# Performance work log

Hardware: AMD Instinct MI355X
Metric: run time of the kernel (lower is better)

Reference implementation:

```python
import jax, jax.numpy as jnp
import numpy as np

D_MODEL = 256      # cfg.d_model
D_INPUT = 64       # cfg.d_input == n_bands
MEM = 10           # cfg.memory_length
NSYNC = 32         # cfg.n_synch_out
ITERS = 2          # cfg.iterations (internal CTM ticks per audio frame)
VOCAB = 15
MINW = 16          # SynapseUNET minimum width; depth=2 -> widths [256, 16]
MHD = 2            # memory_hidden_dims
SYNC_DIM = NSYNC * (NSYNC + 1) // 2  # 528 upper-tri pairwise products


def _ln(x, g, b, eps=1e-5):
    m = x.mean(-1, keepdims=True)
    v = ((x - m) ** 2).mean(-1, keepdims=True)
    return (x - m) * jax.lax.rsqrt(v + eps) * g + b


def _glu(x):
    a, b = jnp.split(x, 2, axis=-1)
    return a * jax.nn.sigmoid(b)


def setup_inputs() -> dict:
    key = jax.random.key(0)
    ks = iter(jax.random.split(key, 40))
    def rn(shape, fan_in):
        return jax.random.uniform(next(ks), shape, jnp.float32, -1.0, 1.0) / np.sqrt(fan_in)
    B, T = 16, 1500
    z = jnp.zeros
    o = jnp.ones
    return {
        "batch_features": jax.random.normal(next(ks), (B, T, D_INPUT), jnp.float32),
        # learned initial traces
        "start_trace": rn((D_MODEL, MEM), MEM),
        "start_activated_trace": rn((D_MODEL, MEM), MEM),
        # classic-control backbone: Linear(64->64) + ReLU
        "Wb": rn((D_INPUT, D_INPUT), D_INPUT), "bb": z((D_INPUT,)),
        # SynapseUNET depth=2, widths [256,16]; input dim = d_input + d_model = 320
        "Wf": rn((D_INPUT + D_MODEL, 2 * D_MODEL), D_INPUT + D_MODEL), "bf": z((2 * D_MODEL,)),
        "gf": o((D_MODEL,)), "bef": z((D_MODEL,)),
        "Wd": rn((D_MODEL, 2 * MINW), D_MODEL), "bd": z((2 * MINW,)),
        "gd": o((MINW,)), "bed": z((MINW,)),
        "Wu": rn((MINW, 2 * D_MODEL), MINW), "bu": z((2 * D_MODEL,)),
        "gu": o((D_MODEL,)), "beu": z((D_MODEL,)),
        "gs": o((D_MODEL,)), "bes": z((D_MODEL,)),
        # deep neuron-level models (per-neuron MLP over the memory trace)
        "w1": rn((MEM, D_MODEL, 2 * MHD), MEM), "b1": z((1, D_MODEL, 2 * MHD)),
        "w2": rn((MHD, D_MODEL, 2), MHD), "b2": z((1, D_MODEL, 2)),
        # output head Linear(528 -> 15)
        "Wh": rn((SYNC_DIM, VOCAB), SYNC_DIM), "bh": z((VOCAB,)),
    }


def reference(batch_features, start_trace, start_activated_trace, Wb, bb,
              Wf, bf, gf, bef, Wd, bd, gd, bed, Wu, bu, gu, beu, gs, bes,
              w1, b1, w2, b2, Wh, bh):
    B = batch_features.shape[0]
    iu, ju = np.triu_indices(NSYNC)  # static index pattern (528 pairs)

    st0 = jnp.broadcast_to(start_trace, (B, D_MODEL, MEM))
    ast0 = jnp.broadcast_to(start_activated_trace, (B, D_MODEL, MEM))

    def synapses(x):  # (B, 320) -> (B, 256), U-Net with one down/up level
        h0 = _ln(_glu(x @ Wf + bf), gf, bef)        # (B, 256)
        d1 = _ln(_glu(h0 @ Wd + bd), gd, bed)       # (B, 16)
        u0 = _ln(_glu(d1 @ Wu + bu), gu, beu)       # (B, 256)
        return _ln(u0 + h0, gs, bes)                # skip + LN

    def nlm(trace):  # per-neuron MLP over memory: (B, 256, 10) -> (B, 256)
        h = _glu(jnp.einsum('bdm,mdh->bdh', trace, w1) + b1)  # (B, 256, 2)
        h = _glu(jnp.einsum('bdm,mdh->bdh', h, w2) + b2)      # (B, 256, 1)
        return h[..., 0]

    def step(carry, x_t):
        st, ast = carry
        kv = jax.nn.relu(x_t @ Wb + bb)  # backbone features (B, 64)
        act = ast[:, :, -1]
        for _ in range(ITERS):  # internal CTM ticks (fixed, small)
            pre = jnp.concatenate([kv, act], axis=-1)             # (B, 320)
            state = synapses(pre)                                  # (B, 256)
            st = jnp.concatenate([st[:, :, 1:], state[:, :, None]], axis=-1)
            act = nlm(st)                                          # (B, 256)
            ast = jnp.concatenate([ast[:, :, 1:], act[:, :, None]], axis=-1)
        sel = act[:, :NSYNC]  # 'first-last': out-sync uses first n_synch_out neurons
        sync = (sel[:, :, None] * sel[:, None, :])[:, iu, ju]      # (B, 528)
        return (st, ast), sync @ Wh + bh                            # (B, 15)

    _, logits = jax.lax.scan(step, (st0, ast0), jnp.swapaxes(batch_features, 0, 1))
    return jnp.swapaxes(logits, 0, 1)  # (B, T, vocab)
```

## Files before the change

### kernel.cpp

```cpp
#include <hip/hip_runtime.h>
#include <math.h>

#define T_LEN 1500
#define DM 256
#define DI 64
#define MEMN 10
#define SYNCD 528
#define VOC 15

typedef _Float16 f16x2 __attribute__((ext_vector_type(2)));
typedef _Float16 f16x8 __attribute__((ext_vector_type(8)));

#define FDOT2(a, b, c) __builtin_amdgcn_fdot2((a), (b), (c), false)

static __device__ __forceinline__ float dot8(f16x8 w, f16x8 q, float acc) {
  acc = FDOT2(__builtin_shufflevector(w, w, 0, 1), __builtin_shufflevector(q, q, 0, 1), acc);
  acc = FDOT2(__builtin_shufflevector(w, w, 2, 3), __builtin_shufflevector(q, q, 2, 3), acc);
  acc = FDOT2(__builtin_shufflevector(w, w, 4, 5), __builtin_shufflevector(q, q, 4, 5), acc);
  acc = FDOT2(__builtin_shufflevector(w, w, 6, 7), __builtin_shufflevector(q, q, 6, 7), acc);
  return acc;
}
static __device__ __forceinline__ f16x2 pack2(float a, float b) {
  f16x2 r; r.x = (_Float16)a; r.y = (_Float16)b; return r;
}
static __device__ __forceinline__ float sigm(float x) { return 1.0f / (1.0f + __expf(-x)); }

struct Params {
  const float *x, *st0, *ast0, *Wb, *bb, *Wf, *bf, *gf, *bef,
              *Wd, *bd, *gd, *bed, *Wu, *bu, *gu, *beu, *gs, *bes,
              *w1, *b1, *w2, *b2, *Wh, *bh;
  float* out;
};

struct Smem {
  float4 W1v[MEMN * DM];
  float4 W2v[DM];
  float4 B1v[DM];
  float2 B2v[DM];
  float Bf[2 * DM];
  float Bu[2 * DM];
  float Bd[32];
  float Gf[DM], Bef[DM], Gu[DM], Beu[DM], Gs[DM], Bes[DM];
  float Gd[16], Bed[16];
  float Bh[16];
  float Bb[DI];
  __attribute__((aligned(16))) float St[MEMN * DM];
  __attribute__((aligned(16))) float H0[DM];
  float Act[DM];
  __attribute__((aligned(16))) float D1[16];
  float X2[2][DI];
  __attribute__((aligned(16))) f16x2 Pre2[160];
  float PartD[16 * 33];
  float PartK[512];
  float PartH[240];
  float2 RedAB[8];
  float2 Red2AB[8];
  float Prod[SYNCD];
  float WhL[SYNCD * VOC];
  int Pair[SYNCD];
};

#define FOR20(X) X(0) X(1) X(2) X(3) X(4) X(5) X(6) X(7) X(8) X(9) \
                 X(10) X(11) X(12) X(13) X(14) X(15) X(16) X(17) X(18) X(19)

#define DECLW(i) f16x8 wa##i, wb##i;
#define LOADW(i) { const float* Wc = P.Wf + (size_t)(p160 + (i) * 8) * 512 + ch; \
  f16x8 ta, tb; \
  _Pragma("unroll") for (int e = 0; e < 8; ++e) { \
    ta[e] = (_Float16)Wc[e * 512]; tb[e] = (_Float16)Wc[e * 512 + 256]; } \
  wa##i = ta; wb##i = tb; }
#define DOT0(i) { f16x8 q = pr8[i]; aA0 = dot8(wa##i, q, aA0); aB0 = dot8(wb##i, q, aB0); }
#define DOT1(i) { f16x8 q = pr8[i]; aA1 = dot8(wa##i, q, aA1); aB1 = dot8(wb##i, q, aB1); }
#define DOTSEQ DOT0(0) DOT1(1) DOT0(2) DOT1(3) DOT0(4) DOT1(5) DOT0(6) DOT1(7) DOT0(8) DOT1(9) \
               DOT0(10) DOT1(11) DOT0(12) DOT1(13) DOT0(14) DOT1(15) DOT0(16) DOT1(17) DOT0(18) DOT1(19)

__global__ __launch_bounds__(512) __attribute__((amdgpu_waves_per_eu(1, 2)))
void ctm_kernel(Params P) {
  const int tid = threadIdx.x;
  const int b = blockIdx.x;
  extern __shared__ char smraw[];
  Smem* sm = (Smem*)smraw;

  for (int i = tid; i < MEMN * DM; i += 512) sm->W1v[i] = ((const float4*)P.w1)[i];
  if (tid < DM) {
    float2 a = ((const float2*)P.w2)[tid];
    float2 c = ((const float2*)P.w2)[DM + tid];
    float4 w; w.x = a.x; w.y = a.y; w.z = c.x; w.w = c.y;
    sm->W2v[tid] = w;
    sm->B1v[tid] = ((const float4*)P.b1)[tid];
    sm->B2v[tid] = ((const float2*)P.b2)[tid];
    sm->Gf[tid] = P.gf[tid]; sm->Bef[tid] = P.bef[tid];
    sm->Gu[tid] = P.gu[tid]; sm->Beu[tid] = P.beu[tid];
    sm->Gs[tid] = P.gs[tid]; sm->Bes[tid] = P.bes[tid];
  }
  sm->Bf[tid] = P.bf[tid];
  sm->Bu[tid] = P.bu[tid];
  if (tid < 32) sm->Bd[tid] = P.bd[tid];
  if (tid < 16) { sm->Gd[tid] = P.gd[tid]; sm->Bed[tid] = P.bed[tid]; }
  if (tid < VOC) sm->Bh[tid] = P.bh[tid];
  if (tid < DI) sm->Bb[tid] = P.bb[tid];
  for (int i = tid; i < MEMN * DM; i += 512) {
    int m = i >> 8, d = i & 255;
    sm->St[m * DM + d] = P.st0[d * MEMN + m];
  }
  if (tid < DI) sm->X2[0][tid] = P.x[(size_t)b * T_LEN * DI + tid];
  for (int i = tid; i < SYNCD * VOC; i += 512) sm->WhL[i] = P.Wh[i];
  for (int pp = tid; pp < SYNCD; pp += 512) {
    int i = 0, cum = 0;
    while (pp >= cum + (32 - i)) { cum += 32 - i; ++i; }
    sm->Pair[pp] = (i << 8) | (i + (pp - cum));
  }

  const int p = tid & 1;
  const int ch = tid >> 1;
  const int p160 = p * 160;
  FOR20(DECLW)
  FOR20(LOADW)
  const int jD = tid & 31, kcD = tid >> 5;
  float wd[16];
  #pragma unroll
  for (int q = 0; q < 16; ++q) wd[q] = P.Wd[(kcD * 16 + q) * 32 + jD];
  float wua[8], wub[8];
  #pragma unroll
  for (int q = 0; q < 8; ++q) {
    wua[q] = P.Wu[(p * 8 + q) * 512 + ch];
    wub[q] = P.Wu[(p * 8 + q) * 512 + ch + 256];
  }
  const int jK = tid & 63, kcK = tid >> 6;
  float wbr[8];
  #pragma unroll
  for (int q = 0; q < 8; ++q) wbr[q] = P.Wb[(kcK * 8 + q) * 64 + jK];

  __syncthreads();

  {
    float s = 0.f;
    #pragma unroll
    for (int q = 0; q < 8; ++q) s += sm->X2[0][kcK * 8 + q] * wbr[q];
    sm->PartK[kcK * 64 + jK] = s;
    if ((tid & 3) == 0) {
      int e = tid >> 2;
      float a0 = P.ast0[(2 * e) * MEMN + (MEMN - 1)];
      float a1 = P.ast0[(2 * e + 1) * MEMN + (MEMN - 1)];
      sm->Pre2[32 + e] = pack2(a0, a1);
    }
  }
  __syncthreads();
  if (tid >= 256 && tid < 320) {
    int j = tid - 256;
    float kv = sm->Bb[j];
    #pragma unroll
    for (int kc = 0; kc < 8; ++kc) kv += sm->PartK[kc * 64 + j];
    kv = fmaxf(kv, 0.f);
    float kn = __shfl_xor(kv, 1);
    if ((j & 1) == 0) sm->Pre2[j >> 1] = pack2(kv, kn);
  }
  __syncthreads();

  int head = 0;
  for (int t = 0; t < T_LEN; ++t) {
    float xr = 0.f;
    if (tid < DI && t + 1 < T_LEN) xr = P.x[((size_t)b * T_LEN + (t + 1)) * DI + tid];

    for (int it = 0; it < 2; ++it) {
      if (it == 1 && tid < DI) sm->X2[(t + 1) & 1][tid] = xr;
      float aA0 = 0.f, aA1 = 0.f, aB0 = 0.f, aB1 = 0.f;
      const f16x8* pr8 = (const f16x8*)(sm->Pre2 + p * 80);
      DOTSEQ
      float av = aA0 + aA1, bv = aB0 + aB1;
      av += __shfl_xor(av, 1); bv += __shfl_xor(bv, 1);
      av += sm->Bf[ch]; bv += sm->Bf[DM + ch];
      float g = av * sigm(bv);
      float s1 = g, s2 = g * g;
      #pragma unroll
      for (int m = 1; m < 64; m <<= 1) { s1 += __shfl_xor(s1, m); s2 += __shfl_xor(s2, m); }
      if ((tid & 63) == 0) { float2 r; r.x = s1; r.y = s2; sm->RedAB[tid >> 6] = r; }
      __syncthreads();

      float S1 = 0.f, S2 = 0.f;
      #pragma unroll
      for (int w = 0; w < 8; ++w) { float2 r = sm->RedAB[w]; S1 += r.x; S2 += r.y; }
      float mean = S1 * (1.0f / 512.0f);
      float var = S2 * (1.0f / 512.0f) - mean * mean;
      float h0v = (g - mean) * rsqrtf(var + 1e-5f) * sm->Gf[ch] + sm->Bef[ch];
      if (!p) sm->H0[ch] = h0v;
      __syncthreads();

      {
        float s = 0.f;
        #pragma unroll
        for (int qq = 0; qq < 4; ++qq) {
          float4 hv = ((const float4*)sm->H0)[kcD * 4 + qq];
          s += hv.x * wd[qq * 4 + 0] + hv.y * wd[qq * 4 + 1]
             + hv.z * wd[qq * 4 + 2] + hv.w * wd[qq * 4 + 3];
        }
        sm->PartD[kcD * 33 + jD] = s;
      }
      __syncthreads();

      if (tid < 32) {
        int j = tid & 15;
        int half = tid >> 4;
        float s = 0.f;
        #pragma unroll
        for (int kc = 0; kc < 16; ++kc) s += sm->PartD[kc * 33 + half * 16 + j];
        float oth = __shfl_xor(s, 16);
        float gg = (s + sm->Bd[j]) * sigm(oth + sm->Bd[16 + j]);
        float t1 = gg, t2 = gg * gg;
        #pragma unroll
        for (int m = 1; m < 16; m <<= 1) { t1 += __shfl_xor(t1, m); t2 += __shfl_xor(t2, m); }
        float mn = t1 * (1.0f / 16.0f), vr = t2 * (1.0f / 16.0f) - mn * mn;
        float d1 = (gg - mn) * rsqrtf(vr + 1e-5f) * sm->Gd[j] + sm->Bed[j];
        if (tid < 16) sm->D1[j] = d1;
      }
      __syncthreads();

      float gu;
      {
        const float4* d4 = (const float4*)sm->D1;
        float4 dl = d4[p * 2], dh = d4[p * 2 + 1];
        float ua = dl.x * wua[0] + dl.y * wua[1] + dl.z * wua[2] + dl.w * wua[3]
                 + dh.x * wua[4] + dh.y * wua[5] + dh.z * wua[6] + dh.w * wua[7];
        float ub = dl.x * wub[0] + dl.y * wub[1] + dl.z * wub[2] + dl.w * wub[3]
                 + dh.x * wub[4] + dh.y * wub[5] + dh.z * wub[6] + dh.w * wub[7];
        ua += __shfl_xor(ua, 1); ub += __shfl_xor(ub, 1);
        ua += sm->Bu[ch]; ub += sm->Bu[DM + ch];
        gu = ua * sigm(ub);
        float t1 = gu, t2 = gu * gu;
        #pragma unroll
        for (int m = 1; m < 64; m <<= 1) { t1 += __shfl_xor(t1, m); t2 += __shfl_xor(t2, m); }
        if ((tid & 63) == 0) { float2 r; r.x = t1; r.y = t2; sm->RedAB[tid >> 6] = r; }
      }
      __syncthreads();

      float x2v;
      {
        float U1 = 0.f, U2 = 0.f;
        #pragma unroll
        for (int w = 0; w < 8; ++w) { float2 r = sm->RedAB[w]; U1 += r.x; U2 += r.y; }
        float mn = U1 * (1.0f / 512.0f), vr = U2 * (1.0f / 512.0f) - mn * mn;
        float u0 = (gu - mn) * rsqrtf(vr + 1e-5f) * sm->Gu[ch] + sm->Beu[ch];
        x2v = u0 + h0v;
        float t1 = x2v, t2 = x2v * x2v;
        #pragma unroll
        for (int m = 1; m < 64; m <<= 1) { t1 += __shfl_xor(t1, m); t2 += __shfl_xor(t2, m); }
        if ((tid & 63) == 0) { float2 r; r.x = t1; r.y = t2; sm->Red2AB[tid >> 6] = r; }
      }
      __syncthreads();

      {
        float V1 = 0.f, V2 = 0.f;
        #pragma unroll
        for (int w = 0; w < 8; ++w) { float2 r = sm->Red2AB[w]; V1 += r.x; V2 += r.y; }
        float mn = V1 * (1.0f / 512.0f), vr = V2 * (1.0f / 512.0f) - mn * mn;
        float state = (x2v - mn) * rsqrtf(vr + 1e-5f) * sm->Gs[ch] + sm->Bes[ch];
        if (!p) sm->St[head * DM + ch] = state;
        float4 h1 = sm->B1v[ch];
        int base = head + 1; if (base >= MEMN) base -= MEMN;
        #pragma unroll
        for (int m = 0; m < MEMN - 1; ++m) {
          int slot = base + m; if (slot >= MEMN) slot -= MEMN;
          float tr = sm->St[slot * DM + ch];
          float4 wv = sm->W1v[m * DM + ch];
          h1.x += tr * wv.x; h1.y += tr * wv.y; h1.z += tr * wv.z; h1.w += tr * wv.w;
        }
        {
          float4 wv = sm->W1v[(MEMN - 1) * DM + ch];
          h1.x += state * wv.x; h1.y += state * wv.y; h1.z += state * wv.z; h1.w += state * wv.w;
        }
        float g0 = h1.x * sigm(h1.z), g1 = h1.y * sigm(h1.w);
        float4 w2v = sm->W2v[ch];
        float2 b2v = sm->B2v[ch];
        float o0 = g0 * w2v.x + g1 * w2v.z + b2v.x;
        float o1 = g0 * w2v.y + g1 * w2v.w + b2v.y;
        float act = o0 * sigm(o1);
        if (!p) sm->Act[ch] = act;
        float an = __shfl_xor(act, 2);
        if ((tid & 3) == 0) sm->Pre2[32 + (tid >> 2)] = pack2(act, an);
        head += 1; if (head >= MEMN) head = 0;
      }
      __syncthreads();
    }

    {
      int pr = sm->Pair[tid];
      sm->Prod[tid] = sm->Act[pr >> 8] * sm->Act[pr & 255];
      if (tid < SYNCD - 512) {
        int pr2 = sm->Pair[512 + tid];
        sm->Prod[512 + tid] = sm->Act[pr2 >> 8] * sm->Act[pr2 & 255];
      }
      const float* X = sm->X2[(t + 1) & 1];
      float s = 0.f;
      #pragma unroll
      for (int q = 0; q < 8; ++q) s += X[kcK * 8 + q] * wbr[q];
      sm->PartK[kcK * 64 + jK] = s;
      if (t > 0 && tid < VOC) {
        float o = sm->Bh[tid];
        #pragma unroll
        for (int kc2 = 0; kc2 < 16; ++kc2) o += sm->PartH[kc2 * 15 + tid];
        P.out[((size_t)b * T_LEN + (t - 1)) * VOC + tid] = o;
      }
    }
    __syncthreads();

    if (tid < 240) {
      int kc = (tid * 4370) >> 16;
      int v = tid - kc * 15;
      float s = 0.f;
      #pragma unroll
      for (int q = 0; q < 33; ++q) {
        int pp = kc * 33 + q;
        s += sm->Prod[pp] * sm->WhL[pp * 15 + v];
      }
      sm->PartH[kc * 15 + v] = s;
    } else if (tid >= 256 && tid < 320) {
      int j = tid - 256;
      float kv = sm->Bb[j];
      #pragma unroll
      for (int kc = 0; kc < 8; ++kc) kv += sm->PartK[kc * 64 + j];
      kv = fmaxf(kv, 0.f);
      float kn = __shfl_xor(kv, 1);
      if ((j & 1) == 0) sm->Pre2[j >> 1] = pack2(kv, kn);
    }
    __syncthreads();
  }

  if (tid < VOC) {
    float o = sm->Bh[tid];
    #pragma unroll
    for (int kc = 0; kc < 16; ++kc) o += sm->PartH[kc * 15 + tid];
    P.out[((size_t)b * T_LEN + (T_LEN - 1)) * VOC + tid] = o;
  }
}

extern "C" void kernel_launch(void* const* d_in, const int* in_sizes, int n_in,
                              void* d_out, int out_size, void* d_ws, size_t ws_size,
                              hipStream_t stream) {
  (void)d_ws; (void)ws_size; (void)n_in; (void)out_size;
  Params P;
  P.x   = (const float*)d_in[0];
  P.st0 = (const float*)d_in[1];
  P.ast0= (const float*)d_in[2];
  P.Wb  = (const float*)d_in[3];
  P.bb  = (const float*)d_in[4];
  P.Wf  = (const float*)d_in[5];
  P.bf  = (const float*)d_in[6];
  P.gf  = (const float*)d_in[7];
  P.bef = (const float*)d_in[8];
  P.Wd  = (const float*)d_in[9];
  P.bd  = (const float*)d_in[10];
  P.gd  = (const float*)d_in[11];
  P.bed = (const float*)d_in[12];
  P.Wu  = (const float*)d_in[13];
  P.bu  = (const float*)d_in[14];
  P.gu  = (const float*)d_in[15];
  P.beu = (const float*)d_in[16];
  P.gs  = (const float*)d_in[17];
  P.bes = (const float*)d_in[18];
  P.w1  = (const float*)d_in[19];
  P.b1  = (const float*)d_in[20];
  P.w2  = (const float*)d_in[21];
  P.b2  = (const float*)d_in[22];
  P.Wh  = (const float*)d_in[23];
  P.bh  = (const float*)d_in[24];
  P.out = (float*)d_out;

  int B = in_sizes[0] / (T_LEN * DI);
  hipFuncSetAttribute((const void*)ctm_kernel, hipFuncAttributeMaxDynamicSharedMemorySize,
                      (int)sizeof(Smem));
  hipLaunchKernelGGL(ctm_kernel, dim3(B), dim3(512), sizeof(Smem), stream, P);
}
```

Baseline: 14.41 ms.

## Double block size to 1024 threads, split each channel's work across four lanes

Each 256-channel synapse row is now split across 4 lanes instead of 2, with the block grown to 1024 threads. Every thread therefore holds half as many Wf f16 weights in registers, and the block-wide reductions and partial-sum arrays are resized to 16 waves. The backbone Wb weights move from registers into shared memory. This shortens the serial per-thread dot-product chain in a latency-bound, sequential-over-time kernel. In exchange it adds extra shuffle reduction steps, more waves taking part in each of the many per-step barriers, and more LDS traffic for Wb.

```diff
diff --git a/kernel.cpp b/kernel.cpp
--- a/kernel.cpp
+++ b/kernel.cpp
@@ -44,44 +44,43 @@
   float Gd[16], Bed[16];
   float Bh[16];
   float Bb[DI];
+  float WbL[DI * DI];
   __attribute__((aligned(16))) float St[MEMN * DM];
   __attribute__((aligned(16))) float H0[DM];
   float Act[DM];
   __attribute__((aligned(16))) float D1[16];
   float X2[2][DI];
   __attribute__((aligned(16))) f16x2 Pre2[160];
-  float PartD[16 * 33];
-  float PartK[512];
+  float PartD[32 * 33];
+  float PartK[16 * 64];
   float PartH[240];
-  float2 RedAB[8];
-  float2 Red2AB[8];
+  float2 RedAB[16];
+  float2 Red2AB[16];
   float Prod[SYNCD];
   float WhL[SYNCD * VOC];
   int Pair[SYNCD];
 };
 
-#define FOR20(X) X(0) X(1) X(2) X(3) X(4) X(5) X(6) X(7) X(8) X(9) \
-                 X(10) X(11) X(12) X(13) X(14) X(15) X(16) X(17) X(18) X(19)
+#define FOR10(X) X(0) X(1) X(2) X(3) X(4) X(5) X(6) X(7) X(8) X(9)
 
 #define DECLW(i) f16x8 wa##i, wb##i;
-#define LOADW(i) { const float* Wc = P.Wf + (size_t)(p160 + (i) * 8) * 512 + ch; \
+#define LOADW(i) { const float* Wc = P.Wf + (size_t)(q80 + (i) * 8) * 512 + ch; \
   f16x8 ta, tb; \
   _Pragma("unroll") for (int e = 0; e < 8; ++e) { \
     ta[e] = (_Float16)Wc[e * 512]; tb[e] = (_Float16)Wc[e * 512 + 256]; } \
   wa##i = ta; wb##i = tb; }
-#define DOT0(i) { f16x8 q = pr8[i]; aA0 = dot8(wa##i, q, aA0); aB0 = dot8(wb##i, q, aB0); }
-#define DOT1(i) { f16x8 q = pr8[i]; aA1 = dot8(wa##i, q, aA1); aB1 = dot8(wb##i, q, aB1); }
-#define DOTSEQ DOT0(0) DOT1(1) DOT0(2) DOT1(3) DOT0(4) DOT1(5) DOT0(6) DOT1(7) DOT0(8) DOT1(9) \
-               DOT0(10) DOT1(11) DOT0(12) DOT1(13) DOT0(14) DOT1(15) DOT0(16) DOT1(17) DOT0(18) DOT1(19)
-
-__global__ __launch_bounds__(512) __attribute__((amdgpu_waves_per_eu(1, 2)))
+#define DOT0(i) { f16x8 qq_ = pr8[i]; aA0 = dot8(wa##i, qq_, aA0); aB0 = dot8(wb##i, qq_, aB0); }
+#define DOT1(i) { f16x8 qq_ = pr8[i]; aA1 = dot8(wa##i, qq_, aA1); aB1 = dot8(wb##i, qq_, aB1); }
+#define DOTSEQ DOT0(0) DOT1(1) DOT0(2) DOT1(3) DOT0(4) DOT1(5) DOT0(6) DOT1(7) DOT0(8) DOT1(9)
+
+__global__ __launch_bounds__(1024)
 void ctm_kernel(Params P) {
   const int tid = threadIdx.x;
   const int b = blockIdx.x;
   extern __shared__ char smraw[];
   Smem* sm = (Smem*)smraw;
 
-  for (int i = tid; i < MEMN * DM; i += 512) sm->W1v[i] = ((const float4*)P.w1)[i];
+  for (int i = tid; i < MEMN * DM; i += 1024) sm->W1v[i] = ((const float4*)P.w1)[i];
   if (tid < DM) {
     float2 a = ((const float2*)P.w2)[tid];
     float2 c = ((const float2*)P.w2)[DM + tid];
@@ -93,64 +92,60 @@
     sm->Gu[tid] = P.gu[tid]; sm->Beu[tid] = P.beu[tid];
     sm->Gs[tid] = P.gs[tid]; sm->Bes[tid] = P.bes[tid];
   }
-  sm->Bf[tid] = P.bf[tid];
-  sm->Bu[tid] = P.bu[tid];
+  if (tid < 2 * DM) { sm->Bf[tid] = P.bf[tid]; sm->Bu[tid] = P.bu[tid]; }
   if (tid < 32) sm->Bd[tid] = P.bd[tid];
   if (tid < 16) { sm->Gd[tid] = P.gd[tid]; sm->Bed[tid] = P.bed[tid]; }
   if (tid < VOC) sm->Bh[tid] = P.bh[tid];
   if (tid < DI) sm->Bb[tid] = P.bb[tid];
-  for (int i = tid; i < MEMN * DM; i += 512) {
+  for (int i = tid; i < DI * DI; i += 1024) sm->WbL[i] = P.Wb[i];
+  for (int i = tid; i < MEMN * DM; i += 1024) {
     int m = i >> 8, d = i & 255;
     sm->St[m * DM + d] = P.st0[d * MEMN + m];
   }
   if (tid < DI) sm->X2[0][tid] = P.x[(size_t)b * T_LEN * DI + tid];
-  for (int i = tid; i < SYNCD * VOC; i += 512) sm->WhL[i] = P.Wh[i];
-  for (int pp = tid; pp < SYNCD; pp += 512) {
+  if (tid < 128) {
+    float a0 = P.ast0[(2 * tid) * MEMN + (MEMN - 1)];
+    float a1 = P.ast0[(2 * tid + 1) * MEMN + (MEMN - 1)];
+    sm->Pre2[32 + tid] = pack2(a0, a1);
+  }
+  for (int i = tid; i < SYNCD * VOC; i += 1024) sm->WhL[i] = P.Wh[i];
+  for (int pp = tid; pp < SYNCD; pp += 1024) {
     int i = 0, cum = 0;
     while (pp >= cum + (32 - i)) { cum += 32 - i; ++i; }
     sm->Pair[pp] = (i << 8) | (i + (pp - cum));
   }
 
-  const int p = tid & 1;
-  const int ch = tid >> 1;
-  const int p160 = p * 160;
-  FOR20(DECLW)
-  FOR20(LOADW)
+  const int q = tid & 3;
+  const int ch = tid >> 2;
+  const int q80 = q * 80;
+  FOR10(DECLW)
+  FOR10(LOADW)
   const int jD = tid & 31, kcD = tid >> 5;
-  float wd[16];
+  float wd[8];
   #pragma unroll
-  for (int q = 0; q < 16; ++q) wd[q] = P.Wd[(kcD * 16 + q) * 32 + jD];
-  float wua[8], wub[8];
+  for (int i = 0; i < 8; ++i) wd[i] = P.Wd[(kcD * 8 + i) * 32 + jD];
+  float wua[4], wub[4];
   #pragma unroll
-  for (int q = 0; q < 8; ++q) {
-    wua[q] = P.Wu[(p * 8 + q) * 512 + ch];
-    wub[q] = P.Wu[(p * 8 + q) * 512 + ch + 256];
+  for (int i = 0; i < 4; ++i) {
+    wua[i] = P.Wu[(q * 4 + i) * 512 + ch];
+    wub[i] = P.Wu[(q * 4 + i) * 512 + ch + 256];
   }
   const int jK = tid & 63, kcK = tid >> 6;
-  float wbr[8];
-  #pragma unroll
-  for (int q = 0; q < 8; ++q) wbr[q] = P.Wb[(kcK * 8 + q) * 64 + jK];
 
   __syncthreads();
 
   {
     float s = 0.f;
     #pragma unroll
-    for (int q = 0; q < 8; ++q) s += sm->X2[0][kcK * 8 + q] * wbr[q];
+    for (int i = 0; i < 4; ++i) s += sm->X2[0][kcK * 4 + i] * sm->WbL[(kcK * 4 + i) * 64 + jK];
     sm->PartK[kcK * 64 + jK] = s;
-    if ((tid & 3) == 0) {
-      int e = tid >> 2;
-      float a0 = P.ast0[(2 * e) * MEMN + (MEMN - 1)];
-      float a1 = P.ast0[(2 * e + 1) * MEMN + (MEMN - 1)];
-      sm->Pre2[32 + e] = pack2(a0, a1);
-    }
   }
   __syncthreads();
   if (tid >= 256 && tid < 320) {
     int j = tid - 256;
     float kv = sm->Bb[j];
     #pragma unroll
-    for (int kc = 0; kc < 8; ++kc) kv += sm->PartK[kc * 64 + j];
+    for (int kc = 0; kc < 16; ++kc) kv += sm->PartK[kc * 64 + j];
     kv = fmaxf(kv, 0.f);
     float kn = __shfl_xor(kv, 1);
     if ((j & 1) == 0) sm->Pre2[j >> 1] = pack2(kv, kn);
@@ -165,10 +160,11 @@
     for (int it = 0; it < 2; ++it) {
       if (it == 1 && tid < DI) sm->X2[(t + 1) & 1][tid] = xr;
       float aA0 = 0.f, aA1 = 0.f, aB0 = 0.f, aB1 = 0.f;
-      const f16x8* pr8 = (const f16x8*)(sm->Pre2 + p * 80);
+      const f16x8* pr8 = (const f16x8*)sm->Pre2 + q * 10;
       DOTSEQ
       float av = aA0 + aA1, bv = aB0 + aB1;
-      av += __shfl_xor(av, 1); bv += __shfl_xor(bv, 1);
+      av += __shfl_xor(av, 1); av += __shfl_xor(av, 2);
+      bv += __shfl_xor(bv, 1); bv += __shfl_xor(bv, 2);
       av += sm->Bf[ch]; bv += sm->Bf[DM + ch];
       float g = av * sigm(bv);
       float s1 = g, s2 = g * g;
@@ -179,18 +175,18 @@
 
       float S1 = 0.f, S2 = 0.f;
       #pragma unroll
-      for (int w = 0; w < 8; ++w) { float2 r = sm->RedAB[w]; S1 += r.x; S2 += r.y; }
-      float mean = S1 * (1.0f / 512.0f);
-      float var = S2 * (1.0f / 512.0f) - mean * mean;
+      for (int w = 0; w < 16; ++w) { float2 r = sm->RedAB[w]; S1 += r.x; S2 += r.y; }
+      float mean = S1 * (1.0f / 1024.0f);
+      float var = S2 * (1.0f / 1024.0f) - mean * mean;
       float h0v = (g - mean) * rsqrtf(var + 1e-5f) * sm->Gf[ch] + sm->Bef[ch];
-      if (!p) sm->H0[ch] = h0v;
+      if (q == 0) sm->H0[ch] = h0v;
       __syncthreads();
 
       {
         float s = 0.f;
         #pragma unroll
-        for (int qq = 0; qq < 4; ++qq) {
-          float4 hv = ((const float4*)sm->H0)[kcD * 4 + qq];
+        for (int qq = 0; qq < 2; ++qq) {
+          float4 hv = ((const float4*)sm->H0)[kcD * 2 + qq];
           s += hv.x * wd[qq * 4 + 0] + hv.y * wd[qq * 4 + 1]
              + hv.z * wd[qq * 4 + 2] + hv.w * wd[qq * 4 + 3];
         }
@@ -198,12 +194,14 @@
       }
       __syncthreads();
 
-      if (tid < 32) {
+      if (tid < 64) {
+        int col = tid & 31;
+        int kh = tid >> 5;
         int j = tid & 15;
-        int half = tid >> 4;
         float s = 0.f;
         #pragma unroll
-        for (int kc = 0; kc < 16; ++kc) s += sm->PartD[kc * 33 + half * 16 + j];
+        for (int i = 0; i < 16; ++i) s += sm->PartD[(kh * 16 + i) * 33 + col];
+        s += __shfl_xor(s, 32);
         float oth = __shfl_xor(s, 16);
         float gg = (s + sm->Bd[j]) * sigm(oth + sm->Bd[16 + j]);
         float t1 = gg, t2 = gg * gg;
@@ -217,13 +215,11 @@
 
       float gu;
       {
-        const float4* d4 = (const float4*)sm->D1;
-        float4 dl = d4[p * 2], dh = d4[p * 2 + 1];
-        float ua = dl.x * wua[0] + dl.y * wua[1] + dl.z * wua[2] + dl.w * wua[3]
-                 + dh.x * wua[4] + dh.y * wua[5] + dh.z * wua[6] + dh.w * wua[7];
-        float ub = dl.x * wub[0] + dl.y * wub[1] + dl.z * wub[2] + dl.w * wub[3]
-                 + dh.x * wub[4] + dh.y * wub[5] + dh.z * wub[6] + dh.w * wub[7];
-        ua += __shfl_xor(ua, 1); ub += __shfl_xor(ub, 1);
+        float4 dl = ((const float4*)sm->D1)[q];
+        float ua = dl.x * wua[0] + dl.y * wua[1] + dl.z * wua[2] + dl.w * wua[3];
+        float ub = dl.x * wub[0] + dl.y * wub[1] + dl.z * wub[2] + dl.w * wub[3];
+        ua += __shfl_xor(ua, 1); ua += __shfl_xor(ua, 2);
+        ub += __shfl_xor(ub, 1); ub += __shfl_xor(ub, 2);
         ua += sm->Bu[ch]; ub += sm->Bu[DM + ch];
         gu = ua * sigm(ub);
         float t1 = gu, t2 = gu * gu;
@@ -237,8 +233,8 @@
       {
         float U1 = 0.f, U2 = 0.f;
         #pragma unroll
-        for (int w = 0; w < 8; ++w) { float2 r = sm->RedAB[w]; U1 += r.x; U2 += r.y; }
-        float mn = U1 * (1.0f / 512.0f), vr = U2 * (1.0f / 512.0f) - mn * mn;
+        for (int w = 0; w < 16; ++w) { float2 r = sm->RedAB[w]; U1 += r.x; U2 += r.y; }
+        float mn = U1 * (1.0f / 1024.0f), vr = U2 * (1.0f / 1024.0f) - mn * mn;
         float u0 = (gu - mn) * rsqrtf(vr + 1e-5f) * sm->Gu[ch] + sm->Beu[ch];
         x2v = u0 + h0v;
         float t1 = x2v, t2 = x2v * x2v;
@@ -251,10 +247,10 @@
       {
         float V1 = 0.f, V2 = 0.f;
         #pragma unroll
-        for (int w = 0; w < 8; ++w) { float2 r = sm->Red2AB[w]; V1 += r.x; V2 += r.y; }
-        float mn = V1 * (1.0f / 512.0f), vr = V2 * (1.0f / 512.0f) - mn * mn;
+        for (int w = 0; w < 16; ++w) { float2 r = sm->Red2AB[w]; V1 += r.x; V2 += r.y; }
+        float mn = V1 * (1.0f / 1024.0f), vr = V2 * (1.0f / 1024.0f) - mn * mn;
         float state = (x2v - mn) * rsqrtf(vr + 1e-5f) * sm->Gs[ch] + sm->Bes[ch];
-        if (!p) sm->St[head * DM + ch] = state;
+        if (q == 0) sm->St[head * DM + ch] = state;
         float4 h1 = sm->B1v[ch];
         int base = head + 1; if (base >= MEMN) base -= MEMN;
         #pragma unroll
@@ -274,25 +270,23 @@
         float o0 = g0 * w2v.x + g1 * w2v.z + b2v.x;
         float o1 = g0 * w2v.y + g1 * w2v.w + b2v.y;
         float act = o0 * sigm(o1);
-        if (!p) sm->Act[ch] = act;
-        float an = __shfl_xor(act, 2);
-        if ((tid & 3) == 0) sm->Pre2[32 + (tid >> 2)] = pack2(act, an);
+        if (q == 0) sm->Act[ch] = act;
+        float an = __shfl_xor(act, 4);
+        if ((tid & 7) == 0) sm->Pre2[32 + (tid >> 3)] = pack2(act, an);
         head += 1; if (head >= MEMN) head = 0;
       }
       __syncthreads();
     }
 
     {
-      int pr = sm->Pair[tid];
-      sm->Prod[tid] = sm->Act[pr >> 8] * sm->Act[pr & 255];
-      if (tid < SYNCD - 512) {
-        int pr2 = sm->Pair[512 + tid];
-        sm->Prod[512 + tid] = sm->Act[pr2 >> 8] * sm->Act[pr2 & 255];
+      if (tid < SYNCD) {
+        int pr = sm->Pair[tid];
+        sm->Prod[tid] = sm->Act[pr >> 8] * sm->Act[pr & 255];
       }
       const float* X = sm->X2[(t + 1) & 1];
       float s = 0.f;
       #pragma unroll
-      for (int q = 0; q < 8; ++q) s += X[kcK * 8 + q] * wbr[q];
+      for (int i = 0; i < 4; ++i) s += X[kcK * 4 + i] * sm->WbL[(kcK * 4 + i) * 64 + jK];
       sm->PartK[kcK * 64 + jK] = s;
       if (t > 0 && tid < VOC) {
         float o = sm->Bh[tid];
@@ -308,8 +302,8 @@
       int v = tid - kc * 15;
       float s = 0.f;
       #pragma unroll
-      for (int q = 0; q < 33; ++q) {
-        int pp = kc * 33 + q;
+      for (int i = 0; i < 33; ++i) {
+        int pp = kc * 33 + i;
         s += sm->Prod[pp] * sm->WhL[pp * 15 + v];
       }
       sm->PartH[kc * 15 + v] = s;
@@ -317,7 +311,7 @@
       int j = tid - 256;
       float kv = sm->Bb[j];
       #pragma unroll
-      for (int kc = 0; kc < 8; ++kc) kv += sm->PartK[kc * 64 + j];
+      for (int kc = 0; kc < 16; ++kc) kv += sm->PartK[kc * 64 + j];
       kv = fmaxf(kv, 0.f);
       float kn = __shfl_xor(kv, 1);
       if ((j & 1) == 0) sm->Pre2[j >> 1] = pack2(kv, kn);
@@ -368,5 +362,5 @@
   int B = in_sizes[0] / (T_LEN * DI);
   hipFuncSetAttribute((const void*)ctm_kernel, hipFuncAttributeMaxDynamicSharedMemorySize,
                       (int)sizeof(Smem));
-  hipLaunchKernelGGL(ctm_kernel, dim3(B), dim3(512), sizeof(Smem), stream, P);
+  hipLaunchKernelGGL(ctm_kernel, dim3(B), dim3(1024), sizeof(Smem), stream, P);
 }
```

Result: slower. 27.31 ms (+89.5%).
